# Kernel optimization log

Measured on AMD Instinct MI355X. Metric: run time of the kernel, lower is better.

Reference implementation:

```python
import jax, jax.numpy as jnp
import numpy as np

GAMMA = 0.9          # EMA momentum for prototype update
N_CLASSES = 201      # 200 classes + 1 background
K_PROTO = 5          # prototypes per class
FG_THRESH = 0.5      # pca_fg_threshold
SK_EPS = 0.05        # sinkhorn temperature (SwAV-style)
SK_ITERS = 3         # sinkhorn iterations
PCA_ITERS = 10       # niter of torch.pca_lowrank


def _l2norm(x, axis=-1):
    return x / jnp.maximum(jnp.linalg.norm(x, axis=axis, keepdims=True), 1e-12)


def _pca_first_component(X, key):
    # Randomized power iteration for the top left singular vector of the
    # centered data (mirrors torch.pca_lowrank(X, q=1, center=True, niter=10)).
    Xc = X - X.mean(0, keepdims=True)            # [N, D]
    G = Xc.T @ Xc                                # [D, D]
    v = jax.random.normal(key, (X.shape[1],), X.dtype)
    v = v / jnp.linalg.norm(v)
    def body(v, _):
        v = G @ v
        return v / jnp.maximum(jnp.linalg.norm(v), 1e-12), None
    v, _ = jax.lax.scan(body, v, None, length=PCA_ITERS)
    u = Xc @ v                                   # [N]
    return u / jnp.maximum(jnp.linalg.norm(u), 1e-12)


def _masked_sinkhorn(logits, mask):
    # logits: [C, BN, K], mask: [C, BN] bool (rows belonging to class c).
    # Vectorized equivalent of the per-class sinkhorn_knopp(L_c): returns a
    # row-stochastic assignment on the masked rows, balanced over the K cols.
    tiny = 1e-9
    m = mask[..., None].astype(logits.dtype)     # [C, BN, 1]
    Q = jnp.exp(logits / SK_EPS) * m
    n_c = jnp.maximum(mask.sum(-1).astype(logits.dtype), 1.0)[:, None, None]
    K = Q.shape[-1]
    Q = Q / jnp.maximum(Q.sum((-2, -1), keepdims=True), tiny)
    for _ in range(SK_ITERS):
        Q = Q / jnp.maximum(Q.sum(-2, keepdims=True), tiny) / K   # balance cols
        Q = Q * m
        Q = Q / jnp.maximum(Q.sum(-1, keepdims=True), tiny) / n_c # balance rows
        Q = Q * m
    return Q * n_c  # each masked row sums to 1


def setup_inputs() -> dict:
    key = jax.random.key(0)
    k1, k2, k3 = jax.random.split(key, 3)
    B, n_patches, dim = 32, 1024, 768
    patch_tokens = jax.random.normal(k1, (B, n_patches, dim), jnp.float32)
    prototypes = 0.02 * jax.random.normal(k2, (N_CLASSES, K_PROTO, dim), jnp.float32)
    labels = jax.random.randint(k3, (B,), 0, 200).astype(jnp.int64)
    return {"patch_tokens": patch_tokens, "prototypes": prototypes, "labels": labels}


def reference(patch_tokens, prototypes, labels):
    B, n_patches, D = patch_tokens.shape

    pt_norm = _l2norm(patch_tokens)              # [B, N, D]
    proto_norm = _l2norm(prototypes)             # [C, K, D]
    # B n_patches dim, C K dim -> B n_patches C K
    logits = jnp.einsum('bnd,ckd->bnck', pt_norm, proto_norm)

    # ---- get_pseudo_patch_labels (PCA foreground extraction) ----
    X = patch_tokens.reshape(-1, D)
    U = _pca_first_component(X, jax.random.key(1))
    U_scaled = (U - U.min()) / (U.max() - U.min())
    fg = (U_scaled < FG_THRESH).reshape(B, n_patches)
    patch_labels = jnp.where(fg, labels[:, None], N_CLASSES - 1)  # [B, N] int

    # ---- update_prototypes, vectorized over the 201-class python loop ----
    pl_flat = patch_labels.reshape(-1)                            # [B*N]
    L = jnp.transpose(logits.reshape(-1, N_CLASSES, K_PROTO), (1, 0, 2))  # [C, BN, K]
    class_ids = jnp.arange(N_CLASSES)
    mask = pl_flat[None, :] == class_ids[:, None]                 # [C, BN]
    Q = _masked_sinkhorn(L, mask)                                 # [C, BN, K]
    # P_c_new = L_c_assignment.T @ I_c, batched over classes
    P_new = jnp.einsum('cnk,nd->ckd', Q, pt_norm.reshape(-1, D))  # [C, K, D]
    present = (labels[None, :] == class_ids[:, None]).any(-1)     # 'c in labels'
    ema = GAMMA * prototypes + (1.0 - GAMMA) * P_new              # momentum_update
    new_prototypes = jnp.where(present[:, None, None], ema, prototypes)

    image_prototype_logits = logits.max(1)        # [B, C, K]
    class_logits = image_prototype_logits.sum(-1) # [B, C]
    return class_logits, image_prototype_logits, new_prototypes
```

## Files before the change

### kernel.cpp

```cpp
#include <hip/hip_runtime.h>
#include <stdint.h>
#include <stddef.h>

#define DEV static __device__ __forceinline__

typedef __attribute__((ext_vector_type(8))) short bf16x8;
typedef __attribute__((ext_vector_type(4))) float f32x4;

DEV float bf2f(unsigned short u){ union{unsigned int i; float f;} v; v.i = ((unsigned int)u)<<16; return v.f; }
DEV unsigned short f2bf(float f){ union{float f; unsigned int i;} v; v.f=f; unsigned int i=v.i;
  return (unsigned short)((i + 0x7FFFu + ((i>>16)&1u)) >> 16); }
DEV unsigned int fenc(float x){ unsigned int i = __float_as_uint(x); return (i & 0x80000000u) ? ~i : (i | 0x80000000u); }
DEV float fdec(unsigned int e){ unsigned int i = (e & 0x80000000u) ? (e & 0x7FFFFFFFu) : ~e; return __uint_as_float(i); }

DEV float waveSum(float s){
  for (int m=32;m;m>>=1) s += __shfl_xor(s, m, 64);
  return s;
}

DEV float blockSum(float v, float* red){
  int t = threadIdx.x;
  red[t] = v; __syncthreads();
  for (int k=128;k>0;k>>=1){ if (t<k) red[t] += red[t+k]; __syncthreads(); }
  float r = red[0]; __syncthreads();
  return r;
}

DEV float erfinv_f(float x){
  float w = -log1pf(-__fmul_rn(x,x));
  float p;
  if (w < 5.0f){
    w = w - 2.5f;
    p = 2.81022636e-08f;
    p = 3.43273939e-07f + p*w;
    p = -3.5233877e-06f + p*w;
    p = -4.39150654e-06f + p*w;
    p = 0.00021858087f + p*w;
    p = -0.00125372503f + p*w;
    p = -0.00417768164f + p*w;
    p = 0.246640727f + p*w;
    p = 1.50140941f + p*w;
  } else {
    w = sqrtf(w) - 3.0f;
    p = -0.000200214257f;
    p = 0.000100950558f + p*w;
    p = 0.00134934322f + p*w;
    p = -0.00367342844f + p*w;
    p = 0.00573950773f + p*w;
    p = -0.0076224613f + p*w;
    p = 0.00943887047f + p*w;
    p = 1.00167406f + p*w;
    p = 2.83297682f + p*w;
  }
  return p*x;
}

#define BN_TOT 32768
#define DIM 768
#define NCLS 201
#define KP 5
#define CKPAD 1024
#define GSPLIT 32
#define PSPLIT 8
#define LPAD 40


__global__ void k_setup(unsigned int* ipl_enc, int* cnt, int* cur, int* present,
                        unsigned int* minmax, float* meansum,
                        const int* __restrict__ raw, int* __restrict__ lab,
                        float* __restrict__ v){
  int i = blockIdx.x*256 + threadIdx.x;
  ipl_enc[i] = 0u;
  if (i < NCLS){ cnt[i]=0; cur[i]=0; present[i]=0; }
  if (i < DIM) meansum[i] = 0.f;
  if (i == 0){
    minmax[0]=0xFFFFFFFFu; minmax[1]=0u;
    bool is64 = true;
    for (int j=0;j<8;j++){
      int lo = raw[2*j], hi = raw[2*j+1];
      if (hi != 0 || lo < 0 || lo >= NCLS-1){ is64 = false; break; }
    }
    for (int j=0;j<32;j++) lab[j] = is64 ? raw[2*j] : raw[j];
  }
  if (i < DIM){
    unsigned int ks[3] = {0u, 1u, 0x1BD11BDBu};
    const int rot0[4] = {13,15,26,6};
    const int rot1[4] = {17,29,16,24};
    unsigned int x0 = 0u, x1 = (unsigned int)i;
    x0 += ks[0]; x1 += ks[1];
    #pragma unroll
    for (int g=0; g<5; g++){
      const int* rr = (g&1) ? rot1 : rot0;
      #pragma unroll
      for (int j=0;j<4;j++){
        x0 += x1;
        x1 = (x1 << rr[j]) | (x1 >> (32-rr[j]));
        x1 ^= x0;
      }
      x0 += ks[(g+1)%3];
      x1 += ks[(g+2)%3] + (unsigned int)(g+1);
    }
    unsigned int b = x0 ^ x1;
    const float lo = __uint_as_float(0xBF7FFFFFu);
    const float sq2 = __uint_as_float(0x3FB504F3u);
    float f = __uint_as_float((b>>9) | 0x3F800000u) - 1.0f;
    float uu = __fadd_rn(__fmul_rn(f, 2.0f), lo);
    uu = fmaxf(lo, uu);
    v[i] = sq2 * erfinv_f(uu);
  }
}

__global__ void k_proto(const float* __restrict__ protos, unsigned short* __restrict__ protn){
  int row = blockIdx.x;
  int l = threadIdx.x;
  if (row >= NCLS*KP){
    for (int j=0;j<12;j++) protn[(size_t)row*DIM + l + j*64] = 0;
    return;
  }
  const float* p = protos + (size_t)row*DIM;
  float x[12]; float s = 0.f;
  for (int j=0;j<12;j++){ x[j] = p[l + j*64]; s += x[j]*x[j]; }
  s = waveSum(s);
  float inv = 1.0f / fmaxf(sqrtf(s), 1e-12f);
  for (int j=0;j<12;j++) protn[(size_t)row*DIM + l + j*64] = f2bf(x[j]*inv);
}

__global__ void k_trans(const float* __restrict__ X, unsigned short* __restrict__ hiT,
                        unsigned short* __restrict__ loT, float* __restrict__ meansum){
  __shared__ float tile[64][65];
  __shared__ float colsum[4][64];
  int n0 = blockIdx.x*64, c0 = blockIdx.y*64;
  int t = threadIdx.x;
  float part = 0.f;
  for (int i=0;i<16;i++){
    int idx = t + i*256; int r = idx>>6, c = idx&63;
    float x = X[(size_t)(n0+r)*DIM + c0+c];
    tile[r][c] = x;
    part += x;
  }
  colsum[t>>6][t&63] = part;
  __syncthreads();
  for (int i=0;i<16;i++){
    int idx = t + i*256; int c = idx>>6, n = idx&63;
    float x = tile[n][c];
    unsigned short h = f2bf(x);
    float hf = bf2f(h);
    unsigned short lo = f2bf(x - hf);
    size_t o = (size_t)(c0+c)*BN_TOT + n0+n;
    hiT[o] = h; loT[o] = lo;
  }
  if (t < 64){
    float s = colsum[0][t]+colsum[1][t]+colsum[2][t]+colsum[3][t];
    atomicAdd(&meansum[c0+t], s);
  }
}

__global__ void k_ptn(const float* __restrict__ X, unsigned short* __restrict__ ptn){
  int row = blockIdx.x*4 + (threadIdx.x>>6);
  int l = threadIdx.x & 63;
  const float* p = X + (size_t)row*DIM;
  float x[12]; float s = 0.f;
  for (int j=0;j<12;j++){ x[j] = p[l + j*64]; s += x[j]*x[j]; }
  s = waveSum(s);
  float inv = 1.0f / fmaxf(sqrtf(s), 1e-12f);
  for (int j=0;j<12;j++) ptn[(size_t)row*DIM + l + j*64] = f2bf(x[j]*inv);
}

__global__ __launch_bounds__(256) void k_gemm_logits(const unsigned short* __restrict__ A,
                                                     const unsigned short* __restrict__ Bt,
                                                     unsigned int* __restrict__ ipl_enc){
  __shared__ __align__(16) unsigned short As[128][LPAD];
  __shared__ __align__(16) unsigned short Bs[128][LPAD];
  __shared__ float red[2][2][64];
  int flat = blockIdx.y*8 + blockIdx.x;
  int xcd = flat & 7, j = flat >> 3;
  int mb = xcd*32 + (j>>3);
  int nb = j & 7;
  int t = threadIdx.x;
  int w = t>>6, l = t&63;
  int wr = w>>1, wc = w&1;
  f32x4 acc[4][4];
  #pragma unroll
  for (int m=0;m<4;m++)
    #pragma unroll
    for (int n=0;n<4;n++){ acc[m][n][0]=0.f; acc[m][n][1]=0.f; acc[m][n][2]=0.f; acc[m][n][3]=0.f; }

  for (int kt=0; kt<24; kt++){
    int k0 = kt*32;
    __syncthreads();
    #pragma unroll
    for (int i=0;i<2;i++){
      int ch = t + i*256;
      int r = ch>>2, co = (ch&3)*8;
      *(uint4*)&As[r][co] = *(const uint4*)&A[(size_t)(mb*128 + r)*DIM + k0 + co];
      *(uint4*)&Bs[r][co] = *(const uint4*)&Bt[(size_t)(nb*128 + r)*DIM + k0 + co];
    }
    __syncthreads();
    bf16x8 a[4], b[4];
    #pragma unroll
    for (int m=0;m<4;m++) a[m] = *(const bf16x8*)&As[wr*64 + m*16 + (l&15)][(l>>4)*8];
    #pragma unroll
    for (int n=0;n<4;n++) b[n] = *(const bf16x8*)&Bs[wc*64 + n*16 + (l&15)][(l>>4)*8];
    #pragma unroll
    for (int m=0;m<4;m++)
      #pragma unroll
      for (int n=0;n<4;n++)
        acc[m][n] = __builtin_amdgcn_mfma_f32_16x16x32_bf16(a[m], b[n], acc[m][n], 0,0,0);
  }
  float vmax[4];
  #pragma unroll
  for (int n=0;n<4;n++){
    float v = -1e30f;
    #pragma unroll
    for (int m=0;m<4;m++)
      #pragma unroll
      for (int r=0;r<4;r++) v = fmaxf(v, acc[m][n][r]);
    v = fmaxf(v, __shfl_xor(v, 16, 64));
    v = fmaxf(v, __shfl_xor(v, 32, 64));
    vmax[n] = v;
  }
  __syncthreads();
  if (l < 16){
    #pragma unroll
    for (int n=0;n<4;n++) red[wc][wr][n*16 + l] = vmax[n];
  }
  __syncthreads();
  if (t < 128){
    int wcc = t>>6, col = t&63;
    float v = fmaxf(red[wcc][0][col], red[wcc][1][col]);
    int gcol = nb*128 + wcc*64 + col;
    if (gcol < NCLS*KP){
      int b = (mb*128) >> 10;
      atomicMax(&ipl_enc[b*CKPAD + gcol], fenc(v));
    }
  }
}

__global__ __launch_bounds__(256) void k_gemm_G(const unsigned short* __restrict__ hiT,
                                                const unsigned short* __restrict__ loT,
                                                float* __restrict__ Gpart){
  __shared__ __align__(16) unsigned short Ahi[128][LPAD];
  __shared__ __align__(16) unsigned short Alo[128][LPAD];
  __shared__ __align__(16) unsigned short Bhi[128][LPAD];
  __shared__ __align__(16) unsigned short Blo[128][LPAD];
  int b = blockIdx.x;
  int xcd = b & 7, q = b >> 3;
  int s = xcd + 8*(q/21);
  int p = q % 21;
  int ib = 0, rem = p;
  while (rem >= 6 - ib){ rem -= 6 - ib; ib++; }
  int jb = ib + rem;
  int t = threadIdx.x, w = t>>6, l = t&63, wr = w>>1, wc = w&1;
  f32x4 acc[4][4];
  #pragma unroll
  for (int m=0;m<4;m++)
    #pragma unroll
    for (int n=0;n<4;n++){ acc[m][n][0]=0.f; acc[m][n][1]=0.f; acc[m][n][2]=0.f; acc[m][n][3]=0.f; }

  for (int kt=0; kt<32; kt++){
    size_t k0 = (size_t)s*1024 + (size_t)kt*32;
    __syncthreads();
    #pragma unroll
    for (int i=0;i<2;i++){
      int ch = t + i*256; int r = ch>>2, co = (ch&3)*8;
      size_t ga = (size_t)(ib*128 + r)*BN_TOT + k0 + co;
      size_t gb = (size_t)(jb*128 + r)*BN_TOT + k0 + co;
      *(uint4*)&Ahi[r][co] = *(const uint4*)&hiT[ga];
      *(uint4*)&Alo[r][co] = *(const uint4*)&loT[ga];
      *(uint4*)&Bhi[r][co] = *(const uint4*)&hiT[gb];
      *(uint4*)&Blo[r][co] = *(const uint4*)&loT[gb];
    }
    __syncthreads();
    bf16x8 ah[4], al[4], bh[4], bl[4];
    #pragma unroll
    for (int m=0;m<4;m++){
      ah[m] = *(const bf16x8*)&Ahi[wr*64 + m*16 + (l&15)][(l>>4)*8];
      al[m] = *(const bf16x8*)&Alo[wr*64 + m*16 + (l&15)][(l>>4)*8];
    }
    #pragma unroll
    for (int n=0;n<4;n++){
      bh[n] = *(const bf16x8*)&Bhi[wc*64 + n*16 + (l&15)][(l>>4)*8];
      bl[n] = *(const bf16x8*)&Blo[wc*64 + n*16 + (l&15)][(l>>4)*8];
    }
    #pragma unroll
    for (int m=0;m<4;m++)
      #pragma unroll
      for (int n=0;n<4;n++){
        acc[m][n] = __builtin_amdgcn_mfma_f32_16x16x32_bf16(ah[m], bh[n], acc[m][n], 0,0,0);
        acc[m][n] = __builtin_amdgcn_mfma_f32_16x16x32_bf16(ah[m], bl[n], acc[m][n], 0,0,0);
        acc[m][n] = __builtin_amdgcn_mfma_f32_16x16x32_bf16(al[m], bh[n], acc[m][n], 0,0,0);
      }
  }
  float* out = Gpart + (size_t)s*DIM*DIM;
  #pragma unroll
  for (int m=0;m<4;m++)
    #pragma unroll
    for (int n=0;n<4;n++)
      #pragma unroll
      for (int r=0;r<4;r++){
        int row = ib*128 + wr*64 + m*16 + (l>>4)*4 + r;
        int col = jb*128 + wc*64 + n*16 + (l&15);
        out[(size_t)row*DIM + col] = acc[m][n][r];
        if (ib != jb) out[(size_t)col*DIM + row] = acc[m][n][r];
      }
}

__global__ void k_gfix(const float* __restrict__ Gpart, const float* __restrict__ meansum,
                       float* __restrict__ G){
  int i = blockIdx.x*256 + threadIdx.x;
  int r = i/DIM, c = i%DIM;
  float s = 0.f;
  for (int p=0;p<GSPLIT;p++) s += Gpart[(size_t)p*DIM*DIM + i];
  const float invN = 1.0f/32768.0f;
  float mr = meansum[r]*invN, mc = meansum[c]*invN;
  G[i] = s*invN - mr*mc;
}

__global__ void k_mv(const float* __restrict__ G, const float* __restrict__ vin,
                     float* __restrict__ vout){
  __shared__ float vs[DIM];
  int t = threadIdx.x;
  for (int i=t;i<DIM;i+=256) vs[i] = vin[i];
  __syncthreads();
  int row = blockIdx.x*4 + (t>>6), l = t&63;
  const float* g = G + (size_t)row*DIM;
  float s = 0.f;
  for (int j=0;j<12;j++) s += g[l + j*64]*vs[l + j*64];
  s = waveSum(s);
  if (l==0) vout[row] = s;
}

__global__ void k_muv(const float* __restrict__ meansum, const float* __restrict__ v,
                      float* __restrict__ scal){
  __shared__ float red[256];
  int t = threadIdx.x;
  float s = 0.f;
  for (int i=t;i<DIM;i+=256) s += meansum[i]*(1.0f/32768.0f)*v[i];
  float r = blockSum(s, red);
  if (t==0) scal[0] = r;
}

__global__ void k_u(const unsigned short* __restrict__ hiT, const unsigned short* __restrict__ loT,
                    const float* __restrict__ v, const float* __restrict__ scal,
                    float* __restrict__ u, unsigned int* __restrict__ minmax){
  __shared__ float vs[DIM];
  int t = threadIdx.x;
  for (int i=t;i<DIM;i+=256) vs[i] = v[i];
  __syncthreads();
  size_t n = (size_t)blockIdx.x*256 + t;
  float acc = 0.f;
  for (int c=0;c<DIM;c++){
    size_t o = (size_t)c*BN_TOT + n;
    acc += (bf2f(hiT[o]) + bf2f(loT[o])) * vs[c];
  }
  float val = acc - scal[0];
  u[n] = val;
  float mn = val, mx = val;
  for (int m=32;m;m>>=1){
    mn = fminf(mn, __shfl_xor(mn, m, 64));
    mx = fmaxf(mx, __shfl_xor(mx, m, 64));
  }
  __shared__ float smn[4], smx[4];
  int w = t>>6;
  if ((t&63)==0){ smn[w]=mn; smx[w]=mx; }
  __syncthreads();
  if (t==0){
    for (int k=1;k<4;k++){ mn = fminf(mn, smn[k]); mx = fmaxf(mx, smx[k]); }
    atomicMin(&minmax[0], fenc(mn));
    atomicMax(&minmax[1], fenc(mx));
  }
}

__global__ void k_pl(const float* __restrict__ u, const int* __restrict__ labels,
                     const unsigned int* __restrict__ minmax, int* __restrict__ pl,
                     int* __restrict__ cnt){
  int n = blockIdx.x*256 + threadIdx.x;
  float umin = fdec(minmax[0]), umax = fdec(minmax[1]);
  float us = (u[n]-umin)/(umax-umin);
  int c = (us < 0.5f) ? labels[n>>10] : (NCLS-1);
  pl[n] = c;
  if (c < NCLS-1) atomicAdd(&cnt[c], 1);
}

__global__ void k_offs(const int* __restrict__ cnt, int* __restrict__ offs,
                       const int* __restrict__ labels, int* __restrict__ present){
  if (threadIdx.x == 0){
    int acc = 0;
    for (int c=0;c<NCLS-1;c++){ offs[c] = acc; acc += cnt[c]; }
    offs[NCLS-1] = acc;
  }
  if (threadIdx.x < 32) atomicOr(&present[labels[threadIdx.x]], 1);
}

__global__ void k_scatter(const int* __restrict__ pl, const int* __restrict__ offs,
                          int* __restrict__ cur, int* __restrict__ idx){
  int n = blockIdx.x*256 + threadIdx.x;
  int c = pl[n];
  if (c < NCLS-1){
    int p = offs[c] + atomicAdd(&cur[c], 1);
    idx[p] = n;
  }
}

__global__ void k_qlog(const int* __restrict__ idx, const int* __restrict__ offs,
                       const int* __restrict__ pl, const unsigned short* __restrict__ ptn,
                       const unsigned short* __restrict__ protn, float* __restrict__ q){
  int i = blockIdx.x*4 + (threadIdx.x>>6);
  int l = threadIdx.x & 63;
  int total = offs[NCLS-1];
  if (i >= total) return;
  int n = idx[i];
  int c = pl[n];
  const unsigned short* pr = ptn + (size_t)n*DIM;
  float x[12];
  for (int j=0;j<12;j++) x[j] = bf2f(pr[l + j*64]);
  for (int k=0;k<KP;k++){
    const unsigned short* wv = protn + (size_t)(c*KP + k)*DIM;
    float s = 0.f;
    for (int j=0;j<12;j++) s += x[j]*bf2f(wv[l + j*64]);
    s = waveSum(s);
    if (l==0) q[(size_t)i*KP + k] = expf(s*20.0f);
  }
}

__global__ void k_sink(const int* __restrict__ cnt, const int* __restrict__ offs,
                       float* __restrict__ q){
  __shared__ float red[256];
  __shared__ float colf[KP];
  int c = blockIdx.x;
  int nc = cnt[c];
  if (nc == 0) return;
  int n0 = offs[c];
  float* Q = q + (size_t)n0*KP;
  int t = threadIdx.x;
  int tot5 = nc*KP;
  float s = 0.f;
  for (int i=t;i<tot5;i+=256) s += Q[i];
  float total = blockSum(s, red);
  float sc = 1.0f/fmaxf(total, 1e-9f);
  for (int i=t;i<tot5;i+=256) Q[i] *= sc;
  __syncthreads();
  float ncf = (float)nc;
  for (int it=0; it<3; it++){
    float cs[KP] = {0,0,0,0,0};
    for (int i=t;i<nc;i+=256){
      const float* row = Q + (size_t)i*KP;
      #pragma unroll
      for (int k=0;k<KP;k++) cs[k] += row[k];
    }
    for (int k=0;k<KP;k++){
      float v = blockSum(cs[k], red);
      if (t==0) colf[k] = 1.0f/(fmaxf(v,1e-9f)*(float)KP);
    }
    __syncthreads();
    for (int i=t;i<nc;i+=256){
      float* row = Q + (size_t)i*KP;
      float qq[KP]; float rs = 0.f;
      #pragma unroll
      for (int k=0;k<KP;k++){ qq[k] = row[k]*colf[k]; rs += qq[k]; }
      float rf = 1.0f/(fmaxf(rs,1e-9f)*ncf);
      #pragma unroll
      for (int k=0;k<KP;k++) row[k] = qq[k]*rf;
    }
    __syncthreads();
  }
  for (int i=t;i<tot5;i+=256) Q[i] *= ncf;
}

__global__ void k_pnew(const int* __restrict__ cnt, const int* __restrict__ offs,
                       const int* __restrict__ present, const int* __restrict__ idx,
                       const float* __restrict__ q, const unsigned short* __restrict__ ptn,
                       float* __restrict__ P4){
  int c = blockIdx.y, s = blockIdx.x;
  if (!present[c]) return;
  int nc = cnt[c], n0 = offs[c];
  int r0 = n0 + (nc*s)/PSPLIT;
  int r1 = n0 + (nc*(s+1))/PSPLIT;
  int t = threadIdx.x;
  float acc[KP][3];
  #pragma unroll
  for (int k=0;k<KP;k++){ acc[k][0]=0.f; acc[k][1]=0.f; acc[k][2]=0.f; }
  for (int i=r0; i<r1; ++i){
    int n = idx[i];
    float qv[KP];
    #pragma unroll
    for (int k=0;k<KP;k++) qv[k] = q[(size_t)i*KP + k];
    const unsigned short* row = ptn + (size_t)n*DIM;
    #pragma unroll
    for (int j=0;j<3;j++){
      float x = bf2f(row[t + j*256]);
      #pragma unroll
      for (int k=0;k<KP;k++) acc[k][j] += qv[k]*x;
    }
  }
  float* out = P4 + ((size_t)(s*NCLS + c)*KP)*DIM;
  #pragma unroll
  for (int k=0;k<KP;k++)
    #pragma unroll
    for (int j=0;j<3;j++)
      out[(size_t)k*DIM + t + j*256] = acc[k][j];
}

__global__ void k_ema(const float* __restrict__ protos, const float* __restrict__ P4,
                      const int* __restrict__ present, float* __restrict__ out){
  int i = blockIdx.x*256 + threadIdx.x;
  if (i >= NCLS*KP*DIM) return;
  int c = i / (KP*DIM);
  float p = protos[i];
  if (present[c]){
    float s = 0.f;
    #pragma unroll
    for (int sp=0; sp<PSPLIT; sp++) s += P4[(size_t)sp*NCLS*KP*DIM + i];
    out[i] = 0.9f*p + 0.1f*s;
  } else {
    out[i] = p;
  }
}

__global__ void k_final(const unsigned int* __restrict__ ipl_enc, float* __restrict__ out){
  int i = blockIdx.x*256 + threadIdx.x;
  if (i < 32*NCLS*KP){
    int b = i / (NCLS*KP), ck = i % (NCLS*KP);
    out[32*NCLS + i] = fdec(ipl_enc[b*CKPAD + ck]);
  }
  if (i < 32*NCLS){
    int b = i / NCLS, c = i % NCLS;
    float s = 0.f;
    #pragma unroll
    for (int k=0;k<KP;k++) s += fdec(ipl_enc[b*CKPAD + c*KP + k]);
    out[b*NCLS + c] = s;
  }
}

extern "C" void kernel_launch(void* const* d_in, const int* in_sizes, int n_in,
                              void* d_out, int out_size, void* d_ws, size_t ws_size,
                              hipStream_t stream){
  (void)in_sizes; (void)n_in; (void)out_size; (void)ws_size;
  const float* X = (const float*)d_in[0];
  const float* protos = (const float*)d_in[1];
  const int* labels_raw = (const int*)d_in[2];
  float* out = (float*)d_out;

  char* w = (char*)d_ws;
  size_t off = 0;
  auto alloc = [&](size_t bytes)->void*{
    void* p = (void*)(w + off);
    off = (off + bytes + 255) & ~(size_t)255;
    return p;
  };
  unsigned short* hiT   = (unsigned short*)alloc((size_t)DIM*BN_TOT*2);
  unsigned short* loT   = (unsigned short*)alloc((size_t)DIM*BN_TOT*2);
  unsigned short* ptn   = (unsigned short*)alloc((size_t)BN_TOT*DIM*2);
  unsigned short* protn = (unsigned short*)alloc((size_t)CKPAD*DIM*2);
  float* Gpart   = (float*)alloc((size_t)GSPLIT*DIM*DIM*4);
  float* G       = (float*)alloc((size_t)DIM*DIM*4);
  float* meansum = (float*)alloc(DIM*4);
  float* vA      = (float*)alloc(DIM*4);
  float* vB      = (float*)alloc(DIM*4);
  float* scal    = (float*)alloc(256);
  int* cnt       = (int*)alloc(1024);
  int* cur       = (int*)alloc(1024);
  int* offs      = (int*)alloc(1024);
  int* present   = (int*)alloc(1024);
  int* labc      = (int*)alloc(256);
  unsigned int* minmax  = (unsigned int*)alloc(256);
  unsigned int* ipl_enc = (unsigned int*)alloc((size_t)32*CKPAD*4);

  {
    char* gb = (char*)Gpart;
    size_t goff = 0;
    auto galloc = [&](size_t bytes)->void*{
      void* p = (void*)(gb + goff);
      goff = (goff + bytes + 255) & ~(size_t)255;
      return p;
    };
    float* u_  = (float*)galloc(BN_TOT*4);
    int* pl_   = (int*)galloc(BN_TOT*4);
    int* idx_  = (int*)galloc(BN_TOT*4);
    float* q_  = (float*)galloc((size_t)BN_TOT*KP*4);
    float* P4_ = (float*)galloc((size_t)PSPLIT*NCLS*KP*DIM*4);

    dim3 b256(256);
    k_setup<<<dim3(128), b256, 0, stream>>>(ipl_enc, cnt, cur, present, minmax, meansum,
                                            labels_raw, labc, vA);
    k_proto<<<dim3(CKPAD), dim3(64), 0, stream>>>(protos, protn);
    k_trans<<<dim3(512,12), b256, 0, stream>>>(X, hiT, loT, meansum);
    k_ptn<<<dim3(8192), b256, 0, stream>>>(X, ptn);
    k_gemm_logits<<<dim3(8,256), b256, 0, stream>>>(ptn, protn, ipl_enc);
    k_gemm_G<<<dim3(21*GSPLIT), b256, 0, stream>>>(hiT, loT, Gpart);
    k_gfix<<<dim3(2304), b256, 0, stream>>>(Gpart, meansum, G);
    for (int it=0; it<10; it++){
      float* src = (it&1) ? vB : vA;
      float* dst = (it&1) ? vA : vB;
      k_mv<<<dim3(192), b256, 0, stream>>>(G, src, dst);
    }
    k_muv<<<dim3(1), b256, 0, stream>>>(meansum, vA, scal);
    k_u<<<dim3(128), b256, 0, stream>>>(hiT, loT, vA, scal, u_, minmax);
    k_pl<<<dim3(128), b256, 0, stream>>>(u_, labc, minmax, pl_, cnt);
    k_offs<<<dim3(1), b256, 0, stream>>>(cnt, offs, labc, present);
    k_scatter<<<dim3(128), b256, 0, stream>>>(pl_, offs, cur, idx_);
    k_qlog<<<dim3(8192), b256, 0, stream>>>(idx_, offs, pl_, ptn, protn, q_);
    k_sink<<<dim3(200), b256, 0, stream>>>(cnt, offs, q_);
    k_pnew<<<dim3(PSPLIT,NCLS), b256, 0, stream>>>(cnt, offs, present, idx_, q_, ptn, P4_);
    k_ema<<<dim3(3015), b256, 0, stream>>>(protos, P4_, present, out + 32*NCLS + 32*NCLS*KP);
    k_final<<<dim3(126), b256, 0, stream>>>(ipl_enc, out);
  }
}
```

Baseline: 528.3 us.

## Use direct-to-LDS loads in G GEMM and fuse small kernels with grid barriers

```diff
diff --git a/kernel.cpp b/kernel.cpp
--- a/kernel.cpp
+++ b/kernel.cpp
@@ -24,6 +24,23 @@
   for (int k=128;k>0;k>>=1){ if (t<k) red[t] += red[t+k]; __syncthreads(); }
   float r = red[0]; __syncthreads();
   return r;
+}
+
+DEV void gl16(const unsigned short* g, unsigned short* lds){
+  __builtin_amdgcn_global_load_lds(
+      (const __attribute__((address_space(1))) void*)g,
+      (__attribute__((address_space(3))) void*)lds, 16, 0, 0);
+}
+
+DEV void gbar(unsigned int* bar, unsigned int target){
+  __syncthreads();
+  if (threadIdx.x==0){
+    __threadfence();
+    atomicAdd(bar, 1u);
+    while (atomicAdd(bar, 0u) < target) __builtin_amdgcn_s_sleep(8);
+    __threadfence();
+  }
+  __syncthreads();
 }
 
 DEV float erfinv_f(float x){
@@ -68,11 +85,12 @@
 __global__ void k_setup(unsigned int* ipl_enc, int* cnt, int* cur, int* present,
                         unsigned int* minmax, float* meansum,
                         const int* __restrict__ raw, int* __restrict__ lab,
-                        float* __restrict__ v){
+                        float* __restrict__ v, unsigned int* bar){
   int i = blockIdx.x*256 + threadIdx.x;
   ipl_enc[i] = 0u;
   if (i < NCLS){ cnt[i]=0; cur[i]=0; present[i]=0; }
   if (i < DIM) meansum[i] = 0.f;
+  if (i < 8) bar[i] = 0u;
   if (i == 0){
     minmax[0]=0xFFFFFFFFu; minmax[1]=0u;
     bool is64 = true;
@@ -236,13 +254,13 @@
   }
 }
 
-__global__ __launch_bounds__(256) void k_gemm_G(const unsigned short* __restrict__ hiT,
+__global__ __launch_bounds__(128) void k_gemm_G(const unsigned short* __restrict__ hiT,
                                                 const unsigned short* __restrict__ loT,
                                                 float* __restrict__ Gpart){
-  __shared__ __align__(16) unsigned short Ahi[128][LPAD];
-  __shared__ __align__(16) unsigned short Alo[128][LPAD];
-  __shared__ __align__(16) unsigned short Bhi[128][LPAD];
-  __shared__ __align__(16) unsigned short Blo[128][LPAD];
+  __shared__ __align__(16) unsigned short Ahi[128*64];
+  __shared__ __align__(16) unsigned short Alo[128*64];
+  __shared__ __align__(16) unsigned short Bhi[128*64];
+  __shared__ __align__(16) unsigned short Blo[128*64];
   int b = blockIdx.x;
   int xcd = b & 7, q = b >> 3;
   int s = xcd + 8*(q/21);
@@ -250,59 +268,78 @@
   int ib = 0, rem = p;
   while (rem >= 6 - ib){ rem -= 6 - ib; ib++; }
   int jb = ib + rem;
-  int t = threadIdx.x, w = t>>6, l = t&63, wr = w>>1, wc = w&1;
-  f32x4 acc[4][4];
+  int t = threadIdx.x, w = t>>6, l = t&63;
+
+  int rl = l>>3;
+  int us = (l&7) ^ (rl&7);
+  size_t lane_off = (size_t)rl*BN_TOT + (size_t)us*8;
+
+  f32x4 acc[8][4];
   #pragma unroll
-  for (int m=0;m<4;m++)
+  for (int m=0;m<8;m++)
     #pragma unroll
     for (int n=0;n<4;n++){ acc[m][n][0]=0.f; acc[m][n][1]=0.f; acc[m][n][2]=0.f; acc[m][n][3]=0.f; }
 
-  for (int kt=0; kt<32; kt++){
-    size_t k0 = (size_t)s*1024 + (size_t)kt*32;
+  #define STAGE_G(KT) { \
+    size_t k0 = (size_t)s*1024 + (size_t)(KT)*64; \
+    _Pragma("unroll") \
+    for (int g=0; g<8; g++){ \
+      int rowg = w + 2*g; \
+      size_t ga = (size_t)(ib*128 + rowg*8)*BN_TOT + k0 + lane_off; \
+      size_t gb = (size_t)(jb*128 + rowg*8)*BN_TOT + k0 + lane_off; \
+      gl16(hiT + ga, Ahi + rowg*512); \
+      gl16(loT + ga, Alo + rowg*512); \
+      gl16(hiT + gb, Bhi + rowg*512); \
+      gl16(loT + gb, Blo + rowg*512); \
+    } }
+
+  STAGE_G(0);
+  for (int kt=0; kt<16; kt++){
+    asm volatile("s_waitcnt vmcnt(0)" ::: "memory");
     __syncthreads();
     #pragma unroll
-    for (int i=0;i<2;i++){
-      int ch = t + i*256; int r = ch>>2, co = (ch&3)*8;
-      size_t ga = (size_t)(ib*128 + r)*BN_TOT + k0 + co;
-      size_t gb = (size_t)(jb*128 + r)*BN_TOT + k0 + co;
-      *(uint4*)&Ahi[r][co] = *(const uint4*)&hiT[ga];
-      *(uint4*)&Alo[r][co] = *(const uint4*)&loT[ga];
-      *(uint4*)&Bhi[r][co] = *(const uint4*)&hiT[gb];
-      *(uint4*)&Blo[r][co] = *(const uint4*)&loT[gb];
+    for (int kk=0; kk<2; kk++){
+      bf16x8 bh[4], bl[4];
+      #pragma unroll
+      for (int n=0;n<4;n++){
+        int r = w*64 + n*16 + (l&15);
+        int phys = (kk*4 + (l>>4)) ^ (r&7);
+        int off = r*64 + phys*8;
+        bh[n] = *(const bf16x8*)&Bhi[off];
+        bl[n] = *(const bf16x8*)&Blo[off];
+      }
+      #pragma unroll
+      for (int m=0;m<8;m++){
+        int r = m*16 + (l&15);
+        int phys = (kk*4 + (l>>4)) ^ (r&7);
+        int off = r*64 + phys*8;
+        bf16x8 ah = *(const bf16x8*)&Ahi[off];
+        bf16x8 al = *(const bf16x8*)&Alo[off];
+        #pragma unroll
+        for (int n=0;n<4;n++){
+          acc[m][n] = __builtin_amdgcn_mfma_f32_16x16x32_bf16(ah, bh[n], acc[m][n], 0,0,0);
+          acc[m][n] = __builtin_amdgcn_mfma_f32_16x16x32_bf16(ah, bl[n], acc[m][n], 0,0,0);
+          acc[m][n] = __builtin_amdgcn_mfma_f32_16x16x32_bf16(al, bh[n], acc[m][n], 0,0,0);
+        }
+      }
     }
     __syncthreads();
-    bf16x8 ah[4], al[4], bh[4], bl[4];
-    #pragma unroll
-    for (int m=0;m<4;m++){
-      ah[m] = *(const bf16x8*)&Ahi[wr*64 + m*16 + (l&15)][(l>>4)*8];
-      al[m] = *(const bf16x8*)&Alo[wr*64 + m*16 + (l&15)][(l>>4)*8];
-    }
-    #pragma unroll
-    for (int n=0;n<4;n++){
-      bh[n] = *(const bf16x8*)&Bhi[wc*64 + n*16 + (l&15)][(l>>4)*8];
-      bl[n] = *(const bf16x8*)&Blo[wc*64 + n*16 + (l&15)][(l>>4)*8];
-    }
-    #pragma unroll
-    for (int m=0;m<4;m++)
-      #pragma unroll
-      for (int n=0;n<4;n++){
-        acc[m][n] = __builtin_amdgcn_mfma_f32_16x16x32_bf16(ah[m], bh[n], acc[m][n], 0,0,0);
-        acc[m][n] = __builtin_amdgcn_mfma_f32_16x16x32_bf16(ah[m], bl[n], acc[m][n], 0,0,0);
-        acc[m][n] = __builtin_amdgcn_mfma_f32_16x16x32_bf16(al[m], bh[n], acc[m][n], 0,0,0);
-      }
-  }
+    if (kt+1 < 16) STAGE_G(kt+1);
+  }
+
   float* out = Gpart + (size_t)s*DIM*DIM;
   #pragma unroll
-  for (int m=0;m<4;m++)
+  for (int m=0;m<8;m++)
     #pragma unroll
     for (int n=0;n<4;n++)
       #pragma unroll
       for (int r=0;r<4;r++){
-        int row = ib*128 + wr*64 + m*16 + (l>>4)*4 + r;
-        int col = jb*128 + wc*64 + n*16 + (l&15);
+        int row = ib*128 + m*16 + (l>>4)*4 + r;
+        int col = jb*128 + w*64 + n*16 + (l&15);
         out[(size_t)row*DIM + col] = acc[m][n][r];
         if (ib != jb) out[(size_t)col*DIM + row] = acc[m][n][r];
       }
+  #undef STAGE_G
 }
 
 __global__ void k_gfix(const float* __restrict__ Gpart, const float* __restrict__ meansum,
@@ -316,28 +353,42 @@
   G[i] = s*invN - mr*mc;
 }
 
-__global__ void k_mv(const float* __restrict__ G, const float* __restrict__ vin,
-                     float* __restrict__ vout){
+__global__ __launch_bounds__(256) void k_power(const float* __restrict__ G,
+                                               float* __restrict__ vA, float* __restrict__ vB,
+                                               const float* __restrict__ meansum,
+                                               float* __restrict__ scal,
+                                               unsigned int* __restrict__ bar){
+  __shared__ float gl[12][DIM];
   __shared__ float vs[DIM];
-  int t = threadIdx.x;
-  for (int i=t;i<DIM;i+=256) vs[i] = vin[i];
-  __syncthreads();
-  int row = blockIdx.x*4 + (t>>6), l = t&63;
-  const float* g = G + (size_t)row*DIM;
-  float s = 0.f;
-  for (int j=0;j<12;j++) s += g[l + j*64]*vs[l + j*64];
-  s = waveSum(s);
-  if (l==0) vout[row] = s;
-}
-
-__global__ void k_muv(const float* __restrict__ meansum, const float* __restrict__ v,
-                      float* __restrict__ scal){
   __shared__ float red[256];
-  int t = threadIdx.x;
-  float s = 0.f;
-  for (int i=t;i<DIM;i+=256) s += meansum[i]*(1.0f/32768.0f)*v[i];
-  float r = blockSum(s, red);
-  if (t==0) scal[0] = r;
+  int t = threadIdx.x, b = blockIdx.x;
+  for (int i=t; i<12*DIM; i+=256){
+    int r = i/DIM, c = i%DIM;
+    gl[r][c] = G[(size_t)(b*12 + r)*DIM + c];
+  }
+  int wv = t>>6, l = t&63;
+  for (int it=0; it<10; it++){
+    const float* src = (it&1) ? vB : vA;
+    float* dst = (it&1) ? vA : vB;
+    for (int i=t;i<DIM;i+=256) vs[i] = src[i];
+    __syncthreads();
+    #pragma unroll
+    for (int rr=0; rr<3; rr++){
+      int row = wv*3 + rr;
+      float s = 0.f;
+      #pragma unroll
+      for (int j=0;j<12;j++) s += gl[row][l + j*64]*vs[l + j*64];
+      s = waveSum(s);
+      if (l==0) dst[b*12 + row] = s;
+    }
+    gbar(bar, 64u*(unsigned)(it+1));
+  }
+  if (b == 0){
+    float s = 0.f;
+    for (int i=t;i<DIM;i+=256) s += meansum[i]*(1.0f/32768.0f)*vA[i];
+    float r = blockSum(s, red);
+    if (t==0) scal[0] = r;
+  }
 }
 
 __global__ void k_u(const unsigned short* __restrict__ hiT, const unsigned short* __restrict__ loT,
@@ -371,33 +422,34 @@
   }
 }
 
-__global__ void k_pl(const float* __restrict__ u, const int* __restrict__ labels,
-                     const unsigned int* __restrict__ minmax, int* __restrict__ pl,
-                     int* __restrict__ cnt){
+__global__ void k_assign(const float* __restrict__ u, const int* __restrict__ labels,
+                         const unsigned int* __restrict__ minmax,
+                         int* __restrict__ pl, int* __restrict__ cnt,
+                         int* __restrict__ offs, int* __restrict__ present,
+                         int* __restrict__ cur, int* __restrict__ idx,
+                         unsigned int* __restrict__ bar){
   int n = blockIdx.x*256 + threadIdx.x;
   float umin = fdec(minmax[0]), umax = fdec(minmax[1]);
   float us = (u[n]-umin)/(umax-umin);
   int c = (us < 0.5f) ? labels[n>>10] : (NCLS-1);
   pl[n] = c;
   if (c < NCLS-1) atomicAdd(&cnt[c], 1);
-}
-
-__global__ void k_offs(const int* __restrict__ cnt, int* __restrict__ offs,
-                       const int* __restrict__ labels, int* __restrict__ present){
-  if (threadIdx.x == 0){
-    int acc = 0;
-    for (int c=0;c<NCLS-1;c++){ offs[c] = acc; acc += cnt[c]; }
-    offs[NCLS-1] = acc;
-  }
-  if (threadIdx.x < 32) atomicOr(&present[labels[threadIdx.x]], 1);
-}
-
-__global__ void k_scatter(const int* __restrict__ pl, const int* __restrict__ offs,
-                          int* __restrict__ cur, int* __restrict__ idx){
-  int n = blockIdx.x*256 + threadIdx.x;
-  int c = pl[n];
+  gbar(bar+1, 128u);
+  if (blockIdx.x == 0){
+    if (threadIdx.x == 0){
+      int acc = 0;
+      for (int cc=0; cc<NCLS-1; cc++){
+        int v = atomicAdd(&cnt[cc], 0);
+        atomicExch(&offs[cc], acc);
+        acc += v;
+      }
+      atomicExch(&offs[NCLS-1], acc);
+    }
+    if (threadIdx.x < 32) atomicOr(&present[labels[threadIdx.x]], 1);
+  }
+  gbar(bar+1, 256u);
   if (c < NCLS-1){
-    int p = offs[c] + atomicAdd(&cur[c], 1);
+    int p = atomicAdd(&offs[c], 0) + atomicAdd(&cur[c], 1);
     idx[p] = n;
   }
 }
@@ -563,46 +615,38 @@
   int* offs      = (int*)alloc(1024);
   int* present   = (int*)alloc(1024);
   int* labc      = (int*)alloc(256);
+  unsigned int* bar     = (unsigned int*)alloc(256);
   unsigned int* minmax  = (unsigned int*)alloc(256);
   unsigned int* ipl_enc = (unsigned int*)alloc((size_t)32*CKPAD*4);
 
-  {
-    char* gb = (char*)Gpart;
-    size_t goff = 0;
-    auto galloc = [&](size_t bytes)->void*{
-      void* p = (void*)(gb + goff);
-      goff = (goff + bytes + 255) & ~(size_t)255;
-      return p;
-    };
-    float* u_  = (float*)galloc(BN_TOT*4);
-    int* pl_   = (int*)galloc(BN_TOT*4);
-    int* idx_  = (int*)galloc(BN_TOT*4);
-    float* q_  = (float*)galloc((size_t)BN_TOT*KP*4);
-    float* P4_ = (float*)galloc((size_t)PSPLIT*NCLS*KP*DIM*4);
-
-    dim3 b256(256);
-    k_setup<<<dim3(128), b256, 0, stream>>>(ipl_enc, cnt, cur, present, minmax, meansum,
-                                            labels_raw, labc, vA);
-    k_proto<<<dim3(CKPAD), dim3(64), 0, stream>>>(protos, protn);
-    k_trans<<<dim3(512,12), b256, 0, stream>>>(X, hiT, loT, meansum);
-    k_ptn<<<dim3(8192), b256, 0, stream>>>(X, ptn);
-    k_gemm_logits<<<dim3(8,256), b256, 0, stream>>>(ptn, protn, ipl_enc);
-    k_gemm_G<<<dim3(21*GSPLIT), b256, 0, stream>>>(hiT, loT, Gpart);
-    k_gfix<<<dim3(2304), b256, 0, stream>>>(Gpart, meansum, G);
-    for (int it=0; it<10; it++){
-      float* src = (it&1) ? vB : vA;
-      float* dst = (it&1) ? vA : vB;
-      k_mv<<<dim3(192), b256, 0, stream>>>(G, src, dst);
-    }
-    k_muv<<<dim3(1), b256, 0, stream>>>(meansum, vA, scal);
-    k_u<<<dim3(128), b256, 0, stream>>>(hiT, loT, vA, scal, u_, minmax);
-    k_pl<<<dim3(128), b256, 0, stream>>>(u_, labc, minmax, pl_, cnt);
-    k_offs<<<dim3(1), b256, 0, stream>>>(cnt, offs, labc, present);
-    k_scatter<<<dim3(128), b256, 0, stream>>>(pl_, offs, cur, idx_);
-    k_qlog<<<dim3(8192), b256, 0, stream>>>(idx_, offs, pl_, ptn, protn, q_);
-    k_sink<<<dim3(200), b256, 0, stream>>>(cnt, offs, q_);
-    k_pnew<<<dim3(PSPLIT,NCLS), b256, 0, stream>>>(cnt, offs, present, idx_, q_, ptn, P4_);
-    k_ema<<<dim3(3015), b256, 0, stream>>>(protos, P4_, present, out + 32*NCLS + 32*NCLS*KP);
-    k_final<<<dim3(126), b256, 0, stream>>>(ipl_enc, out);
-  }
-}
+  char* gb = (char*)Gpart;
+  size_t goff = 0;
+  auto galloc = [&](size_t bytes)->void*{
+    void* p = (void*)(gb + goff);
+    goff = (goff + bytes + 255) & ~(size_t)255;
+    return p;
+  };
+  float* u_  = (float*)galloc(BN_TOT*4);
+  int* pl_   = (int*)galloc(BN_TOT*4);
+  int* idx_  = (int*)galloc(BN_TOT*4);
+  float* q_  = (float*)galloc((size_t)BN_TOT*KP*4);
+  float* P4_ = (float*)galloc((size_t)PSPLIT*NCLS*KP*DIM*4);
+
+  dim3 b256(256);
+  k_setup<<<dim3(128), b256, 0, stream>>>(ipl_enc, cnt, cur, present, minmax, meansum,
+                                          labels_raw, labc, vA, bar);
+  k_proto<<<dim3(CKPAD), dim3(64), 0, stream>>>(protos, protn);
+  k_trans<<<dim3(512,12), b256, 0, stream>>>(X, hiT, loT, meansum);
+  k_ptn<<<dim3(8192), b256, 0, stream>>>(X, ptn);
+  k_gemm_logits<<<dim3(8,256), b256, 0, stream>>>(ptn, protn, ipl_enc);
+  k_gemm_G<<<dim3(21*GSPLIT), dim3(128), 0, stream>>>(hiT, loT, Gpart);
+  k_gfix<<<dim3(2304), b256, 0, stream>>>(Gpart, meansum, G);
+  k_power<<<dim3(64), b256, 0, stream>>>(G, vA, vB, meansum, scal, bar);
+  k_u<<<dim3(128), b256, 0, stream>>>(hiT, loT, vA, scal, u_, minmax);
+  k_assign<<<dim3(128), b256, 0, stream>>>(u_, labc, minmax, pl_, cnt, offs, present, cur, idx_, bar);
+  k_qlog<<<dim3(8192), b256, 0, stream>>>(idx_, offs, pl_, ptn, protn, q_);
+  k_sink<<<dim3(200), b256, 0, stream>>>(cnt, offs, q_);
+  k_pnew<<<dim3(PSPLIT,NCLS), b256, 0, stream>>>(cnt, offs, present, idx_, q_, ptn, P4_);
+  k_ema<<<dim3(3015), b256, 0, stream>>>(protos, P4_, present, out + 32*NCLS + 32*NCLS*KP);
+  k_final<<<dim3(126), b256, 0, stream>>>(ipl_enc, out);
+}
```

Result: slower. 596.4 us (+12.9%).
